# Optimization experiments

Measured on AMD Instinct MI355X. Metric: run time of the kernel, lower is better.

## Reference

```python
import jax, jax.numpy as jnp
import numpy as np

B, C, H, W = 8, 512, 64, 64
S = 64
STD = 0.001  # torch init.normal_(weight, std=0.001)


def setup_inputs() -> dict:
    key = jax.random.key(0)
    ks = jax.random.split(key, 7)
    return {
        "queries": jax.random.normal(ks[0], (B, C, H, W), dtype=jnp.float32),
        "k": jax.random.normal(ks[1], (B, C, H, W), dtype=jnp.float32),
        "v": jax.random.normal(ks[2], (B, C, H, W), dtype=jnp.float32),
        "Wq": jax.random.normal(ks[3], (S, C), dtype=jnp.float32) * STD,
        "Wk": jax.random.normal(ks[4], (S, C), dtype=jnp.float32) * STD,
        "Wv": jax.random.normal(ks[5], (S, C), dtype=jnp.float32) * STD,
        "Wl": jax.random.normal(ks[6], (C, S), dtype=jnp.float32) * STD,
    }


def _branch(A, Bp, Cp, Wl):
    # A,Bp,Cp: [h,w,b,S] projected tensors
    m = jnp.einsum('hwbs,hwbt->hwst', A, Bp)          # [h,w,S,S]
    m = jax.nn.softmax(m, axis=1)                      # softmax over w (dim=1, as in torch)
    o = jnp.einsum('hwst,hwbt->hwsb', m, Cp)           # [h,w,S,b]
    o = o / jnp.sum(o, axis=2, keepdims=True)          # normalize over S
    o = jnp.einsum('hwsb,cs->hwbc', o, Wl)             # transpose + Linear(S->C)
    return jnp.transpose(o, (2, 3, 0, 1))              # [b,c,h,w]


def reference(queries, k, v, Wq, Wk, Wv, Wl):
    q = jnp.transpose(queries, (2, 3, 0, 1))  # [h,w,b,c]
    kk = jnp.transpose(k, (2, 3, 0, 1))
    vv = jnp.transpose(v, (2, 3, 0, 1))
    aq = jnp.einsum('hwbc,sc->hwbs', q, Wq)   # [h,w,b,S]
    ak = jnp.einsum('hwbc,sc->hwbs', kk, Wk)
    av = jnp.einsum('hwbc,sc->hwbs', vv, Wv)
    out_q = _branch(aq, ak, av, Wl)
    out_k = _branch(ak, av, aq, Wl)
    out_v = _branch(av, aq, ak, Wl)
    return jnp.concatenate((out_q, out_k, out_v), axis=0)  # [3b,c,h,w]
```

## Files before the change

### kernel.cpp

```cpp
#include <hip/hip_runtime.h>
#include <hip/hip_bf16.h>

#define HW 4096
#define CCH 512
#define SDIM 64
#define BDIM 8

typedef __attribute__((ext_vector_type(8))) short short8;
typedef __attribute__((ext_vector_type(4))) float f32x4;

static __device__ __forceinline__ ushort f2bf(float f) {
  __hip_bfloat16 h = __float2bfloat16(f);
  return *reinterpret_cast<ushort*>(&h);
}
static __device__ __forceinline__ float bf2f(ushort u) {
  union { unsigned int u32; float f; } c;
  c.u32 = ((unsigned int)u) << 16;
  return c.f;
}
static __device__ __forceinline__ ushort trunc_bf(float f, float* rem) {
  union { float f; unsigned int u; } a; a.f = f;
  union { float f; unsigned int u; } h; h.u = a.u & 0xFFFF0000u;
  *rem = f - h.f;
  return (ushort)(a.u >> 16);
}
static __device__ __forceinline__ ushort rne_bf(float f) {
  union { float f; unsigned int u; } a; a.f = f;
  return (ushort)((a.u + 0x8000u) >> 16);
}
static __device__ __forceinline__ void gll16(const void* g, void* lds_base) {
  __builtin_amdgcn_global_load_lds(
      (const __attribute__((address_space(1))) unsigned int*)g,
      (__attribute__((address_space(3))) unsigned int*)lds_base, 16, 0, 0);
}

__global__ __launch_bounds__(256) void prep_kernel(const float* __restrict__ Wq,
                                                   const float* __restrict__ Wk,
                                                   const float* __restrict__ Wv,
                                                   const float* __restrict__ Wl,
                                                   ushort* __restrict__ whi,
                                                   ushort* __restrict__ wmid,
                                                   ushort* __restrict__ wlo,
                                                   ushort* __restrict__ wlhi,
                                                   ushort* __restrict__ wllo) {
  const int idx = blockIdx.x * 1024 + threadIdx.x * 4;
  if (blockIdx.y == 3) {
    float4 f = *reinterpret_cast<const float4*>(&Wl[idx]);
    ushort4 h, l;
    float r;
    h.x = trunc_bf(f.x, &r); l.x = rne_bf(r);
    h.y = trunc_bf(f.y, &r); l.y = rne_bf(r);
    h.z = trunc_bf(f.z, &r); l.z = rne_bf(r);
    h.w = trunc_bf(f.w, &r); l.w = rne_bf(r);
    *reinterpret_cast<ushort4*>(&wlhi[idx]) = h;
    *reinterpret_cast<ushort4*>(&wllo[idx]) = l;
    return;
  }
  const float* W = blockIdx.y == 0 ? Wq : (blockIdx.y == 1 ? Wk : Wv);
  float4 f = *reinterpret_cast<const float4*>(&W[idx]);
  ushort4 h, m, l;
  float r, r2;
  h.x = f2bf(f.x); r = f.x - bf2f(h.x); m.x = f2bf(r); r2 = r - bf2f(m.x); l.x = f2bf(r2);
  h.y = f2bf(f.y); r = f.y - bf2f(h.y); m.y = f2bf(r); r2 = r - bf2f(m.y); l.y = f2bf(r2);
  h.z = f2bf(f.z); r = f.z - bf2f(h.z); m.z = f2bf(r); r2 = r - bf2f(m.z); l.z = f2bf(r2);
  h.w = f2bf(f.w); r = f.w - bf2f(h.w); m.w = f2bf(r); r2 = r - bf2f(m.w); l.w = f2bf(r2);
  const size_t o = (size_t)blockIdx.y * (SDIM * CCH) + idx;
  *reinterpret_cast<ushort4*>(&whi[o])  = h;
  *reinterpret_cast<ushort4*>(&wmid[o]) = m;
  *reinterpret_cast<ushort4*>(&wlo[o])  = l;
}

__global__ __launch_bounds__(256) void proj_mfma_kernel(const float* __restrict__ q,
                                                        const float* __restrict__ k,
                                                        const float* __restrict__ v,
                                                        const ushort* __restrict__ whi,
                                                        const ushort* __restrict__ wmid,
                                                        const ushort* __restrict__ wlo,
                                                        float* __restrict__ ap) {
  __shared__ float Xs[2][32 * 128];
  __shared__ ushort Ws[2][3][64 * 32];
  const int mt = blockIdx.x;
  const int b = blockIdx.y;
  const int br = blockIdx.z;
  const float* x = br == 0 ? q : (br == 1 ? k : v);
  const ushort* wsrc[3] = {whi + (size_t)br * SDIM * CCH,
                           wmid + (size_t)br * SDIM * CCH,
                           wlo + (size_t)br * SDIM * CCH};
  float* apo = ap + (size_t)br * HW * 512;
  const int hw0 = mt * 128;
  const int tid = threadIdx.x;
  const int l = tid & 63;
  const int wid = tid >> 6;
  const int wstrip = wid * 32;
  const int row16 = l & 15;
  const int kgrp = l >> 4;
  const float* xcol = x + (size_t)b * CCH * HW + hw0;
  const int rbase = 8 * wid;
  const int rsub = l >> 5;
  const int wrow = wid * 16 + (l >> 2);
  const int wblk = (l & 3) ^ ((l >> 3) & 3);
  const int jp = kgrp ^ ((row16 >> 1) & 3);
  const int xswz = (kgrp & 1) << 4;

  f32x4 acc_hi[2][4] = {};
  f32x4 acc_co[2][4] = {};

#define STAGE(BUF, CI)                                                            \
  do {                                                                            \
                      \
    _Pragma("unroll") for (int j = 0; j < 4; ++j) {                               \
      const int r = rbase + 2 * j + rsub;                                         \
      const int hwsrc = (((l & 31) ^ ((((r) >> 3) & 1) << 2)) * 4);               \
      gll16(xcol + (size_t)((CI) * 32 + r) * HW + hwsrc,                          \
            &Xs[BUF][(rbase + 2 * j) * 128]);                                     \
    }                                                                             \
                            \
    _Pragma("unroll") for (int lv = 0; lv < 3; ++lv)                              \
      gll16(wsrc[lv] + (size_t)wrow * CCH + (CI) * 32 + wblk * 8,                 \
            &Ws[BUF][lv][wid * 512]);                                             \
  } while (0)

  STAGE(0, 0);

  for (int ci = 0; ci < 16; ++ci) {
    __builtin_amdgcn_sched_barrier(0);
    if (ci < 15) {
      STAGE((ci + 1) & 1, ci + 1);
      __builtin_amdgcn_sched_barrier(0);
      asm volatile("s_waitcnt vmcnt(7)" ::: "memory");
    } else {
      asm volatile("s_waitcnt vmcnt(0)" ::: "memory");
    }
    __builtin_amdgcn_sched_barrier(0);
    __builtin_amdgcn_s_barrier();
    __builtin_amdgcn_sched_barrier(0);

    short8 bh[4], bm[4], bl[4];
#pragma unroll
    for (int nf = 0; nf < 4; ++nf) {
      const int woff = (nf * 16 + row16) * 32 + jp * 8;
      bh[nf] = *reinterpret_cast<const short8*>(&Ws[ci & 1][0][woff]);
      bm[nf] = *reinterpret_cast<const short8*>(&Ws[ci & 1][1][woff]);
      bl[nf] = *reinterpret_cast<const short8*>(&Ws[ci & 1][2][woff]);
    }

    const float* lw = &Xs[ci & 1][0];
#pragma unroll
    for (int mf = 0; mf < 2; ++mf) {
      const int rowA = (wstrip + mf * 16 + row16) ^ xswz;
      short8 ah, am, al;
      {
        ushort th[8], tm[8], tl[8];
#pragma unroll
        for (int i = 0; i < 8; ++i) {
          const float f = lw[(kgrp * 8 + i) * 128 + rowA];
          float r, r2;
          th[i] = trunc_bf(f, &r);
          tm[i] = trunc_bf(r, &r2);
          tl[i] = rne_bf(r2);
        }
        ah = *reinterpret_cast<const short8*>(th);
        am = *reinterpret_cast<const short8*>(tm);
        al = *reinterpret_cast<const short8*>(tl);
      }
#pragma unroll
      for (int nf = 0; nf < 4; ++nf) {
        acc_hi[mf][nf] = __builtin_amdgcn_mfma_f32_16x16x32_bf16(ah, bh[nf], acc_hi[mf][nf], 0, 0, 0);
        acc_co[mf][nf] = __builtin_amdgcn_mfma_f32_16x16x32_bf16(ah, bm[nf], acc_co[mf][nf], 0, 0, 0);
        acc_co[mf][nf] = __builtin_amdgcn_mfma_f32_16x16x32_bf16(am, bh[nf], acc_co[mf][nf], 0, 0, 0);
        acc_co[mf][nf] = __builtin_amdgcn_mfma_f32_16x16x32_bf16(am, bm[nf], acc_co[mf][nf], 0, 0, 0);
        acc_co[mf][nf] = __builtin_amdgcn_mfma_f32_16x16x32_bf16(ah, bl[nf], acc_co[mf][nf], 0, 0, 0);
        acc_co[mf][nf] = __builtin_amdgcn_mfma_f32_16x16x32_bf16(al, bh[nf], acc_co[mf][nf], 0, 0, 0);
        acc_co[mf][nf] = __builtin_amdgcn_mfma_f32_16x16x32_bf16(am, bl[nf], acc_co[mf][nf], 0, 0, 0);
        acc_co[mf][nf] = __builtin_amdgcn_mfma_f32_16x16x32_bf16(al, bm[nf], acc_co[mf][nf], 0, 0, 0);
      }
    }
    __builtin_amdgcn_sched_barrier(0);
    __builtin_amdgcn_s_barrier();
    __builtin_amdgcn_sched_barrier(0);
  }
#undef STAGE

#pragma unroll
  for (int mf = 0; mf < 2; ++mf)
#pragma unroll
    for (int nf = 0; nf < 4; ++nf)
#pragma unroll
      for (int r = 0; r < 4; ++r) {
        const int m = hw0 + wstrip + mf * 16 + kgrp * 4 + r;
        apo[(size_t)m * 512 + b * 64 + nf * 16 + row16] = acc_hi[mf][nf][r] + acc_co[mf][nf][r];
      }
}

__global__ __launch_bounds__(512) void denom_kernel(const float* __restrict__ ap,
                                                    float* __restrict__ rD) {
  __shared__ float As[8 * 16];
  __shared__ float Bs[8 * 64];
  const int h = blockIdx.x, br = blockIdx.y, sq = blockIdx.z;
  const float* A  = ap + ((size_t)br * HW + (size_t)h * 64) * (BDIM * SDIM);
  const float* Bp = ap + ((size_t)((br + 1) % 3) * HW + (size_t)h * 64) * (BDIM * SDIM);
  const int tid = threadIdx.x;
  const int t = tid & 63;
  const int sg = tid >> 6;
  float D[2] = {};
  for (int w = 0; w < 64; ++w) {
    __syncthreads();
    if (tid < 128) As[tid] = A[w * 512 + (tid >> 4) * 64 + sq * 16 + (tid & 15)];
    Bs[tid] = Bp[w * 512 + tid];
    __syncthreads();
    float bv[8];
#pragma unroll
    for (int b = 0; b < 8; ++b) bv[b] = Bs[b * 64 + t];
#pragma unroll
    for (int j = 0; j < 2; ++j) {
      const int sl = sg * 2 + j;
      float m = 0.f;
#pragma unroll
      for (int b = 0; b < 8; ++b) m = fmaf(As[b * 16 + sl], bv[b], m);
      D[j] += __expf(m);
    }
  }
#pragma unroll
  for (int j = 0; j < 2; ++j)
    rD[((size_t)(br * 64 + h) * 64 + sq * 16 + sg * 2 + j) * 64 + t] = 1.0f / D[j];
}

__global__ __launch_bounds__(256) void attn_kernel(const float* __restrict__ ap,
                                                   const float* __restrict__ rD,
                                                   float* __restrict__ on) {
  __shared__ float As[8 * 64], Bs[8 * 64], Cs[8 * 64];
  __shared__ float Ms[64 * 65];
  const int wc = blockIdx.x, h = blockIdx.y, br = blockIdx.z;
  const float* A  = ap + ((size_t)br * HW + h * 64) * 512;
  const float* Bp = ap + ((size_t)((br + 1) % 3) * HW + h * 64) * 512;
  const float* Cp = ap + ((size_t)((br + 2) % 3) * HW + h * 64) * 512;
  const float* rDp = rD + (size_t)(br * 64 + h) * 4096;
  const int tid = threadIdx.x;
  for (int w = wc * 8; w < wc * 8 + 8; ++w) {
    __syncthreads();
#pragma unroll
    for (int it = 0; it < 2; ++it) {
      int idx = it * 256 + tid;
      As[idx] = A[w * 512 + idx];
      Bs[idx] = Bp[w * 512 + idx];
      Cs[idx] = Cp[w * 512 + idx];
    }
    __syncthreads();
    {
      const int t = tid & 63, sg = tid >> 6;
      float bv[8];
#pragma unroll
      for (int b = 0; b < 8; ++b) bv[b] = Bs[b * 64 + t];
#pragma unroll
      for (int j = 0; j < 16; ++j) {
        int s = sg * 16 + j;
        float m = 0.f;
#pragma unroll
        for (int b = 0; b < 8; ++b) m = fmaf(As[b * 64 + s], bv[b], m);
        Ms[t * 65 + s] = __expf(m) * rDp[s * 64 + t];
      }
    }
    __syncthreads();
    const int s2 = tid & 63, bq = tid >> 6;
    float o0 = 0.f, o1 = 0.f;
#pragma unroll
    for (int tt = 0; tt < 64; tt += 4) {
      const float m0 = Ms[(tt + 0) * 65 + s2];
      const float m1 = Ms[(tt + 1) * 65 + s2];
      const float m2 = Ms[(tt + 2) * 65 + s2];
      const float m3 = Ms[(tt + 3) * 65 + s2];
      float4 c0 = *reinterpret_cast<const float4*>(&Cs[bq * 64 + tt]);
      float4 c1 = *reinterpret_cast<const float4*>(&Cs[(bq + 4) * 64 + tt]);
      o0 = fmaf(m3, c0.w, fmaf(m2, c0.z, fmaf(m1, c0.y, fmaf(m0, c0.x, o0))));
      o1 = fmaf(m3, c1.w, fmaf(m2, c1.z, fmaf(m1, c1.y, fmaf(m0, c1.x, o1))));
    }
    float n0 = o0, n1 = o1;
#pragma unroll
    for (int off = 32; off > 0; off >>= 1) {
      n0 += __shfl_xor(n0, off);
      n1 += __shfl_xor(n1, off);
    }
    const float r0 = 1.0f / n0, r1 = 1.0f / n1;
    const size_t ob = ((size_t)br * HW + h * 64 + w) * 512;
    on[ob + (size_t)bq * 64 + s2] = o0 * r0;
    on[ob + (size_t)(bq + 4) * 64 + s2] = o1 * r1;
  }
}

__global__ __launch_bounds__(256) void out_kernel(const float* __restrict__ on,
                                                  const ushort* __restrict__ wlhi,
                                                  const ushort* __restrict__ wllo,
                                                  float* __restrict__ out) {
  __shared__ float Os[128 * 68];
  const int hwt = blockIdx.x;
  const int brb = blockIdx.y;
  const int br = brb >> 3, b = brb & 7;
  const int hw0 = hwt * 128;
  const int tid = threadIdx.x;
  const int l = tid & 63;
  const int wv = tid >> 6;
  const int l15 = l & 15;
  const int kgrp = l >> 4;

  {
    const int row = tid >> 4;
    const int s4 = (tid & 15) * 4;
#pragma unroll
    for (int it = 0; it < 8; ++it) {
      const int r = row + it * 16;
      *reinterpret_cast<float4*>(&Os[r * 68 + s4]) =
          *reinterpret_cast<const float4*>(&on[((size_t)(br * HW + hw0 + r) * 8 + b) * 64 + s4]);
    }
  }
  __syncthreads();

  short8 onh[2][2], onl[2][2];
#pragma unroll
  for (int nf = 0; nf < 2; ++nf)
#pragma unroll
    for (int ks = 0; ks < 2; ++ks) {
      const int row = wv * 32 + nf * 16 + l15;
      const float* p = &Os[row * 68 + ks * 32 + kgrp * 8];
      ushort th[8], tl[8];
#pragma unroll
      for (int i = 0; i < 8; ++i) {
        float r;
        th[i] = trunc_bf(p[i], &r);
        tl[i] = rne_bf(r);
      }
      onh[nf][ks] = *reinterpret_cast<const short8*>(th);
      onl[nf][ks] = *reinterpret_cast<const short8*>(tl);
    }

  for (int mf = 0; mf < 32; ++mf) {
    f32x4 acc[2] = {};
#pragma unroll
    for (int ks = 0; ks < 2; ++ks) {
      const size_t woff = (size_t)(mf * 16 + l15) * 64 + ks * 32 + kgrp * 8;
      const short8 wh8 = *reinterpret_cast<const short8*>(&wlhi[woff]);
      const short8 wl8 = *reinterpret_cast<const short8*>(&wllo[woff]);
#pragma unroll
      for (int nf = 0; nf < 2; ++nf) {
        acc[nf] = __builtin_amdgcn_mfma_f32_16x16x32_bf16(wh8, onh[nf][ks], acc[nf], 0, 0, 0);
        acc[nf] = __builtin_amdgcn_mfma_f32_16x16x32_bf16(wh8, onl[nf][ks], acc[nf], 0, 0, 0);
        acc[nf] = __builtin_amdgcn_mfma_f32_16x16x32_bf16(wl8, onh[nf][ks], acc[nf], 0, 0, 0);
      }
    }
#pragma unroll
    for (int nf = 0; nf < 2; ++nf)
#pragma unroll
      for (int r = 0; r < 4; ++r) {
        const int cc = mf * 16 + kgrp * 4 + r;
        out[(size_t)(brb * 512 + cc) * HW + hw0 + wv * 32 + nf * 16 + l15] = acc[nf][r];
      }
  }
}

extern "C" void kernel_launch(void* const* d_in, const int* in_sizes, int n_in,
                              void* d_out, int out_size, void* d_ws, size_t ws_size,
                              hipStream_t stream) {
  const float* q  = (const float*)d_in[0];
  const float* k  = (const float*)d_in[1];
  const float* v  = (const float*)d_in[2];
  const float* Wq = (const float*)d_in[3];
  const float* Wk = (const float*)d_in[4];
  const float* Wv = (const float*)d_in[5];
  const float* Wl = (const float*)d_in[6];
  float* out = (float*)d_out;

  float* ap = (float*)d_ws;
  float* rD = ap + (size_t)3 * HW * 512;
  float* on = rD + (size_t)3 * 64 * 64 * 64;
  ushort* whi  = (ushort*)rD;
  ushort* wmid = whi + (size_t)3 * SDIM * CCH;
  ushort* wlo  = wmid + (size_t)3 * SDIM * CCH;
  ushort* wlhi = (ushort*)(on + (size_t)3 * HW * 512);
  ushort* wllo = wlhi + (size_t)SDIM * CCH;

  prep_kernel<<<dim3(32, 4), 256, 0, stream>>>(Wq, Wk, Wv, Wl, whi, wmid, wlo, wlhi, wllo);
  proj_mfma_kernel<<<dim3(32, 8, 3), 256, 0, stream>>>(q, k, v, whi, wmid, wlo, ap);
  denom_kernel<<<dim3(64, 3, 4), 512, 0, stream>>>(ap, rD);
  attn_kernel<<<dim3(8, 64, 3), 256, 0, stream>>>(ap, rD, on);
  out_kernel<<<dim3(32, 24), 256, 0, stream>>>(on, wlhi, wllo, out);
}
```

Before: 250.8 us.

## Pipeline attention tile loads with triple-buffered async global-to-LDS copies

The attention kernel now stages each w-column's A/B/C tiles through a triple-buffered LDS ring using direct global-to-LDS loads, prefetching the next column while computing the current one. Each tile is loaded by one of three waves. The per-thread row-normalisation factors (rD) are now loaded into registers once per block instead of being reread from global memory every iteration. This is meant to hide global load latency and cut redundant loads. It relies on manual vmcnt waits and barriers being correct, and the extra rdv registers may lower occupancy.

Result: faster. 239.4 us (-4.6%).

```diff
diff --git a/kernel.cpp b/kernel.cpp
--- a/kernel.cpp
+++ b/kernel.cpp
@@ -107,14 +107,12 @@
 
 #define STAGE(BUF, CI)                                                            \
   do {                                                                            \
-                      \
     _Pragma("unroll") for (int j = 0; j < 4; ++j) {                               \
       const int r = rbase + 2 * j + rsub;                                         \
       const int hwsrc = (((l & 31) ^ ((((r) >> 3) & 1) << 2)) * 4);               \
       gll16(xcol + (size_t)((CI) * 32 + r) * HW + hwsrc,                          \
             &Xs[BUF][(rbase + 2 * j) * 128]);                                     \
     }                                                                             \
-                            \
     _Pragma("unroll") for (int lv = 0; lv < 3; ++lv)                              \
       gll16(wsrc[lv] + (size_t)wrow * CCH + (CI) * 32 + wblk * 8,                 \
             &Ws[BUF][lv][wid * 512]);                                             \
@@ -228,7 +226,7 @@
 __global__ __launch_bounds__(256) void attn_kernel(const float* __restrict__ ap,
                                                    const float* __restrict__ rD,
                                                    float* __restrict__ on) {
-  __shared__ float As[8 * 64], Bs[8 * 64], Cs[8 * 64];
+  __shared__ float Tile[3][3 * 512];
   __shared__ float Ms[64 * 65];
   const int wc = blockIdx.x, h = blockIdx.y, br = blockIdx.z;
   const float* A  = ap + ((size_t)br * HW + h * 64) * 512;
@@ -236,41 +234,69 @@
   const float* Cp = ap + ((size_t)((br + 2) % 3) * HW + h * 64) * 512;
   const float* rDp = rD + (size_t)(br * 64 + h) * 4096;
   const int tid = threadIdx.x;
-  for (int w = wc * 8; w < wc * 8 + 8; ++w) {
-    __syncthreads();
-#pragma unroll
-    for (int it = 0; it < 2; ++it) {
-      int idx = it * 256 + tid;
-      As[idx] = A[w * 512 + idx];
-      Bs[idx] = Bp[w * 512 + idx];
-      Cs[idx] = Cp[w * 512 + idx];
-    }
-    __syncthreads();
+  const int t = tid & 63;
+  const int sg = tid >> 6;
+  const int w0 = wc * 8;
+
+  float rdv[16];
+#pragma unroll
+  for (int j = 0; j < 16; ++j) rdv[j] = rDp[(sg * 16 + j) * 64 + t];
+
+  const float* src = sg == 0 ? A : (sg == 1 ? Bp : Cp);
+
+#define STAGE_T(BUF, W)                                                   \
+  do {                                                                    \
+    if (sg < 3) {                                                         \
+      _Pragma("unroll") for (int j = 0; j < 2; ++j)                       \
+        gll16(src + (size_t)(W) * 512 + j * 256 + t * 4,                  \
+              &Tile[BUF][sg * 512 + j * 256]);                            \
+    }                                                                     \
+  } while (0)
+
+  STAGE_T(0, w0);
+
+  for (int wi = 0; wi < 8; ++wi) {
+    __builtin_amdgcn_sched_barrier(0);
+    if (wi < 7) {
+      STAGE_T((wi + 1) % 3, w0 + wi + 1);
+      __builtin_amdgcn_sched_barrier(0);
+      asm volatile("s_waitcnt vmcnt(2)" ::: "memory");
+    } else {
+      asm volatile("s_waitcnt vmcnt(0)" ::: "memory");
+    }
+    __builtin_amdgcn_sched_barrier(0);
+    __builtin_amdgcn_s_barrier();
+    __builtin_amdgcn_sched_barrier(0);
+
+    const float* Aw = &Tile[wi % 3][0];
+    const float* Bw = &Tile[wi % 3][512];
+    const float* Cw = &Tile[wi % 3][1024];
     {
-      const int t = tid & 63, sg = tid >> 6;
       float bv[8];
 #pragma unroll
-      for (int b = 0; b < 8; ++b) bv[b] = Bs[b * 64 + t];
+      for (int b = 0; b < 8; ++b) bv[b] = Bw[b * 64 + t];
 #pragma unroll
       for (int j = 0; j < 16; ++j) {
-        int s = sg * 16 + j;
+        const int s = sg * 16 + j;
         float m = 0.f;
 #pragma unroll
-        for (int b = 0; b < 8; ++b) m = fmaf(As[b * 64 + s], bv[b], m);
-        Ms[t * 65 + s] = __expf(m) * rDp[s * 64 + t];
-      }
-    }
-    __syncthreads();
-    const int s2 = tid & 63, bq = tid >> 6;
+        for (int b = 0; b < 8; ++b) m = fmaf(Aw[b * 64 + s], bv[b], m);
+        Ms[t * 65 + s] = __expf(m) * rdv[j];
+      }
+    }
+    __builtin_amdgcn_sched_barrier(0);
+    __builtin_amdgcn_s_barrier();
+    __builtin_amdgcn_sched_barrier(0);
+
     float o0 = 0.f, o1 = 0.f;
 #pragma unroll
     for (int tt = 0; tt < 64; tt += 4) {
-      const float m0 = Ms[(tt + 0) * 65 + s2];
-      const float m1 = Ms[(tt + 1) * 65 + s2];
-      const float m2 = Ms[(tt + 2) * 65 + s2];
-      const float m3 = Ms[(tt + 3) * 65 + s2];
-      float4 c0 = *reinterpret_cast<const float4*>(&Cs[bq * 64 + tt]);
-      float4 c1 = *reinterpret_cast<const float4*>(&Cs[(bq + 4) * 64 + tt]);
+      const float m0 = Ms[(tt + 0) * 65 + t];
+      const float m1 = Ms[(tt + 1) * 65 + t];
+      const float m2 = Ms[(tt + 2) * 65 + t];
+      const float m3 = Ms[(tt + 3) * 65 + t];
+      float4 c0 = *reinterpret_cast<const float4*>(&Cw[sg * 64 + tt]);
+      float4 c1 = *reinterpret_cast<const float4*>(&Cw[(sg + 4) * 64 + tt]);
       o0 = fmaf(m3, c0.w, fmaf(m2, c0.z, fmaf(m1, c0.y, fmaf(m0, c0.x, o0))));
       o1 = fmaf(m3, c1.w, fmaf(m2, c1.z, fmaf(m1, c1.y, fmaf(m0, c1.x, o1))));
     }
@@ -281,10 +307,11 @@
       n1 += __shfl_xor(n1, off);
     }
     const float r0 = 1.0f / n0, r1 = 1.0f / n1;
-    const size_t ob = ((size_t)br * HW + h * 64 + w) * 512;
-    on[ob + (size_t)bq * 64 + s2] = o0 * r0;
-    on[ob + (size_t)(bq + 4) * 64 + s2] = o1 * r1;
-  }
+    const size_t ob = ((size_t)br * HW + h * 64 + w0 + wi) * 512;
+    on[ob + (size_t)sg * 64 + t] = o0 * r0;
+    on[ob + (size_t)(sg + 4) * 64 + t] = o1 * r1;
+  }
+#undef STAGE_T
 }
 
 __global__ __launch_bounds__(256) void out_kernel(const float* __restrict__ on,
```
